# Kernel tuning notes

Measured on AMD Instinct MI355X. Metric: run time of the kernel, lower is better.

Reference implementation:

```python
import jax, jax.numpy as jnp
import numpy as np

INPUT_SIZE = 512
HIDDEN = 1024
N_QP = 64
M_QP = 128
QP_ITER = 50
MIN_EIG = 0.01
N_P = N_QP * (N_QP + 1) // 2              # 2080
N_H = M_QP * N_QP                          # 8192
N_OUT = N_P + N_QP + N_H + M_QP            # 10464
BATCH = 1024


def setup_inputs() -> dict:
    key = jax.random.key(0)
    ks = jax.random.split(key, 4)
    s = lambda fan_in: np.float32(1.0 / np.sqrt(fan_in))
    return {
        "x": jax.random.normal(ks[0], (BATCH, INPUT_SIZE), jnp.float32),
        "W1": jax.random.normal(ks[1], (INPUT_SIZE, HIDDEN), jnp.float32) * s(INPUT_SIZE),
        "b1": jnp.zeros((HIDDEN,), jnp.float32),
        "W2": jax.random.normal(ks[2], (HIDDEN, HIDDEN), jnp.float32) * s(HIDDEN),
        "b2": jnp.zeros((HIDDEN,), jnp.float32),
        "W3": jax.random.normal(ks[3], (HIDDEN, N_OUT), jnp.float32) * s(HIDDEN),
        "b3": jnp.zeros((N_OUT,), jnp.float32),
    }


def _make_psd(p):
    # p: (bs, n(n+1)/2) packed row-major lower triangle of Cholesky factor L.
    # Diagonal entries (index i(i+1)/2 - 1) -> sqrt(min_eig) + softplus, so P = L L' is PSD.
    bs = p.shape[0]
    i = jnp.arange(1, N_QP + 1)
    diag_idx = i * (i + 1) // 2 - 1
    p = p.at[:, diag_idx].set(np.float32(np.sqrt(MIN_EIG)) + jax.nn.softplus(p[:, diag_idx]))
    r, c = jnp.tril_indices(N_QP)
    L = jnp.zeros((bs, N_QP, N_QP), p.dtype).at[:, r, c].set(p)
    return jnp.einsum('bik,bjk->bij', L, L)


def _forward(x, W1, b1, W2, b2, W3, b3):
    # MLP generating QP parameters (P, q, H, b)
    h = jax.nn.relu(x @ W1 + b1)
    h = jax.nn.relu(h @ W2 + b2)
    out = h @ W3 + b3                               # (bs, N_OUT)
    P_params = out[:, :N_P]
    q = out[:, N_P:N_P + N_QP]                      # (bs, n)
    H = out[:, N_P + N_QP:N_P + N_QP + N_H].reshape(-1, M_QP, N_QP)  # (bs, m, n)
    b = out[:, N_P + N_QP + N_H:]                   # (bs, m)
    P = _make_psd(P_params)                         # (bs, n, n)

    # Step sizes: tau = sigma = 0.9 / ||H||_2, spectral norm via 10 fixed power iterations
    v = jnp.ones((x.shape[0], N_QP), x.dtype) / np.float32(np.sqrt(N_QP))
    for _ in range(10):
        w = jnp.einsum('bmn,bm->bn', H, jnp.einsum('bmn,bn->bm', H, v))
        v = w / (jnp.linalg.norm(w, axis=1, keepdims=True) + 1e-12)
    sn = jnp.linalg.norm(jnp.einsum('bmn,bn->bm', H, v), axis=1) + 1e-6
    tau = (0.9 / sn)[:, None]                       # (bs, 1) primal step
    sig = tau                                       # dual step

    # Precompute (I + tau P)^{-1} once; fixed across PDHG iterations
    eye = jnp.eye(N_QP, dtype=x.dtype)
    Minv = jnp.linalg.inv(eye[None] + tau[:, :, None] * P)

    x0 = jnp.zeros((x.shape[0], N_QP), x.dtype)
    lam0 = jnp.zeros((x.shape[0], M_QP), x.dtype)

    def step(carry, _):
        xp, xbar, lam = carry
        lam = jax.nn.relu(lam - sig * (jnp.einsum('bmn,bn->bm', H, xbar) + b))
        xn = jnp.einsum('bnk,bk->bn', Minv, xp + tau * (jnp.einsum('bmn,bm->bn', H, lam) - q))
        return (xn, 2.0 * xn - xp, lam), None

    (xs, _, _), _ = jax.lax.scan(step, (x0, x0, lam0), None, length=QP_ITER)
    return xs  # (bs, n_qp): last primal iterate, matching solver(...)[1][:, -1, :]


def reference(x, W1, b1, W2, b2, W3, b3):
    return _forward(x, W1, b1, W2, b2, W3, b3)
```

## Files before the change

### kernel.cpp

```cpp
#include <hip/hip_runtime.h>
#include <cstdint>

typedef unsigned short u16;
typedef __attribute__((ext_vector_type(8))) short short8;
typedef __attribute__((ext_vector_type(4))) float floatx4;
typedef __attribute__((ext_vector_type(4))) float f4;

#define NQP   64
#define MQP   128
#define NP    2080
#define NHH   8192
#define NOUT  10464
#define NOUTP 10496

__device__ __forceinline__ float b2f(u16 u) {
  union { unsigned int i; float f; } v; v.i = ((unsigned int)u) << 16; return v.f;
}
__device__ __forceinline__ u16 f2b(float f) {
  union { float f; unsigned int i; } v; v.f = f;
  unsigned int r = v.i + 0x7fffu + ((v.i >> 16) & 1u);
  return (u16)(r >> 16);
}

__global__ __launch_bounds__(256) void detect_dtype(const u16* __restrict__ w,
                                                    int* __restrict__ flag) {
  __shared__ int cnt;
  if (threadIdx.x == 0) cnt = 0;
  __syncthreads();
  int c = 0;
  for (int i = threadIdx.x; i < 16384; i += 256) {
    const int e = (w[i] >> 7) & 0xFF;
    if (e >= 130 || e <= 90) ++c;
  }
  atomicAdd(&cnt, c);
  __syncthreads();
  if (threadIdx.x == 0) flag[0] = (cnt > 3000) ? 1 : 0;
}

__device__ __forceinline__ u16 load_elem_bf16(const void* p, size_t idx, int isf32) {
  return isf32 ? f2b(((const float*)p)[idx]) : ((const u16*)p)[idx];
}

__global__ __launch_bounds__(256) void convert_bf16(const void* __restrict__ in,
                                                    u16* __restrict__ out, int n,
                                                    const int* __restrict__ flag) {
  const int isf = flag[0];
  for (int i = blockIdx.x * 256 + threadIdx.x; i < n; i += gridDim.x * 256)
    out[i] = load_elem_bf16(in, i, isf);
}

__global__ __launch_bounds__(256) void conv_biases(const void* __restrict__ b1,
                                                   const void* __restrict__ b2,
                                                   const void* __restrict__ b3,
                                                   float* __restrict__ bf1,
                                                   float* __restrict__ bf2,
                                                   float* __restrict__ bf3,
                                                   const int* __restrict__ flag) {
  const int isf = flag[0];
  const int i = blockIdx.x * 256 + threadIdx.x;
  if (i < 1024) {
    bf1[i] = isf ? ((const float*)b1)[i] : b2f(((const u16*)b1)[i]);
  } else if (i < 2048) {
    const int j = i - 1024;
    bf2[j] = isf ? ((const float*)b2)[j] : b2f(((const u16*)b2)[j]);
  } else if (i < 2048 + NOUT) {
    const int j = i - 2048;
    bf3[j] = isf ? ((const float*)b3)[j] : b2f(((const u16*)b3)[j]);
  }
}

__global__ __launch_bounds__(256) void transpose_all(const void* __restrict__ W1,
                                                     const void* __restrict__ W2,
                                                     const void* __restrict__ W3,
                                                     u16* __restrict__ W1t,
                                                     u16* __restrict__ W2t,
                                                     u16* __restrict__ W3t,
                                                     const int* __restrict__ flag) {
  const int bx = blockIdx.x, by = blockIdx.y;
  const void* in; u16* out; int K, N, Npad, bxo;
  if (bx < 32)      { in = W1; out = W1t; K = 512;  N = 1024; Npad = 1024;  bxo = 0;
                      if (by >= 16) return; }
  else if (bx < 64) { in = W2; out = W2t; K = 1024; N = 1024; Npad = 1024;  bxo = 32; }
  else              { in = W3; out = W3t; K = 1024; N = NOUT; Npad = NOUTP; bxo = 64; }
  __shared__ u16 tile[32][33];
  const int isf = flag[0];
  const int n0 = (bx - bxo) * 32, k0 = by * 32;
  const int tx = threadIdx.x & 31, ty = threadIdx.x >> 5;
#pragma unroll
  for (int i = 0; i < 4; ++i) {
    const int k = k0 + ty + 8 * i, n = n0 + tx;
    tile[ty + 8 * i][tx] = (n < N) ? load_elem_bf16(in, (size_t)k * N + n, isf) : (u16)0;
  }
  __syncthreads();
#pragma unroll
  for (int i = 0; i < 4; ++i) {
    const int n = n0 + ty + 8 * i, k = k0 + tx;
    if (n < Npad) out[(size_t)n * K + k] = tile[tx][ty + 8 * i];
  }
}

__device__ __forceinline__ void gload_lds16(const u16* g, u16* l) {
  __builtin_amdgcn_global_load_lds((const __attribute__((address_space(1))) void*)g,
                                   (__attribute__((address_space(3))) void*)l, 16, 0, 0);
}

template <int EPI, bool HAS_LO>
__global__ __launch_bounds__(256) void gemm_bt(const u16* __restrict__ Ahi, const u16* __restrict__ Alo,
                                               const u16* __restrict__ Bt,  const float* __restrict__ bias,
                                               u16* __restrict__ Chi, u16* __restrict__ Clo,
                                               float* __restrict__ Cf,
                                               int M, int N, int K) {
  __shared__ __align__(16) u16 lA[128 * 32];
  __shared__ __align__(16) u16 lAlo[128 * 32];
  __shared__ __align__(16) u16 lB[128 * 32];
  const int tile_n = blockIdx.x * 128;
  const int tile_m = blockIdx.y * 128;
  const int lane = threadIdx.x & 63;
  const int wv   = threadIdx.x >> 6;
  const int wm = (wv & 1) * 64;
  const int wn = (wv >> 1) * 64;
  const int sr = lane >> 2;
  const int sk = (lane & 3) * 8;
  floatx4 acc[4][4] = {};

  for (int k0 = 0; k0 < K; k0 += 32) {
#pragma unroll
    for (int it = 0; it < 2; ++it) {
      const int slot = it * 4 + wv;
      const int r = slot * 16 + sr;
      gload_lds16(Ahi + (size_t)(tile_m + r) * K + k0 + sk, lA + slot * 512);
      if (HAS_LO)
        gload_lds16(Alo + (size_t)(tile_m + r) * K + k0 + sk, lAlo + slot * 512);
      gload_lds16(Bt + (size_t)(tile_n + r) * K + k0 + sk, lB + slot * 512);
    }
    __syncthreads();
    const int ro = lane & 15;
    const int qo = (lane >> 4) * 8;
    short8 af[4], bfr[4], al[4];
#pragma unroll
    for (int i = 0; i < 4; ++i) af[i] = *(const short8*)(lA + (wm + i * 16 + ro) * 32 + qo);
#pragma unroll
    for (int j = 0; j < 4; ++j) bfr[j] = *(const short8*)(lB + (wn + j * 16 + ro) * 32 + qo);
    if (HAS_LO) {
#pragma unroll
      for (int i = 0; i < 4; ++i) al[i] = *(const short8*)(lAlo + (wm + i * 16 + ro) * 32 + qo);
    }
#pragma unroll
    for (int i = 0; i < 4; ++i)
#pragma unroll
      for (int j = 0; j < 4; ++j) {
        acc[i][j] = __builtin_amdgcn_mfma_f32_16x16x32_bf16(af[i], bfr[j], acc[i][j], 0, 0, 0);
        if (HAS_LO)
          acc[i][j] = __builtin_amdgcn_mfma_f32_16x16x32_bf16(al[i], bfr[j], acc[i][j], 0, 0, 0);
      }
    __syncthreads();
  }

  const int colb = tile_n + wn + (lane & 15);
  const int rowb = tile_m + wm + (lane >> 4) * 4;
#pragma unroll
  for (int j = 0; j < 4; ++j) {
    const int col = colb + j * 16;
    const float bv = (col < N) ? bias[col] : 0.f;
#pragma unroll
    for (int i = 0; i < 4; ++i) {
#pragma unroll
      for (int v = 0; v < 4; ++v) {
        const int row = rowb + i * 16 + v;
        float val = acc[i][j][v] + bv;
        if (EPI == 0) {
          val = fmaxf(val, 0.f);
          const u16 hi = f2b(val);
          const float lo = val - b2f(hi);
          Chi[(size_t)row * N + col] = hi;
          Clo[(size_t)row * N + col] = f2b(lo);
        } else if (EPI == 2) {
          val = fmaxf(val, 0.f);
          Chi[(size_t)row * N + col] = f2b(val);
        } else {
          if (col < N) Cf[(size_t)row * N + col] = val;
        }
      }
    }
  }
}

__device__ __forceinline__ f4 ld4s(const float* p) { return *(const f4*)p; }
__device__ __forceinline__ void st4s(float* p, f4 v) { *(f4*)p = v; }
__device__ __forceinline__ float dot4(f4 a, f4 b) {
  return fmaf(a.x, b.x, fmaf(a.y, b.y, fmaf(a.z, b.z, a.w * b.w)));
}
__device__ __forceinline__ f4 shx4(f4 v, int m) {
  f4 r;
  r.x = __shfl_xor(v.x, m, 64); r.y = __shfl_xor(v.y, m, 64);
  r.z = __shfl_xor(v.z, m, 64); r.w = __shfl_xor(v.w, m, 64);
  return r;
}
__device__ __forceinline__ int hQ(int m, int g) {
  return (m << 6) + (((g ^ (m & 15))) << 2);
}

__global__ __launch_bounds__(256, 4) void qp_solve(const float* __restrict__ outbuf,
                                                   void* __restrict__ xs,
                                                   const int* __restrict__ flag) {
  __shared__ __align__(16) float H_s[8192];
  __shared__ __align__(16) float lam_s[128];
  __shared__ __align__(16) float b_s[128];
  __shared__ __align__(16) float part_s[4][64];
  __shared__ __align__(16) float rhs_s[64];
  __shared__ __align__(16) float xb_s[64];
  __shared__ __align__(16) float xp_s[64];
  __shared__ __align__(16) float q_s[64];
  __shared__ __align__(16) float buf2[2][64];
  __shared__ float tau_sh;

  const int t = threadIdx.x;
  const int w = t >> 6, l = t & 63;
  const int am = 32 * w + (l >> 1), as = l & 1;
  const int bg = l & 15, bc = l >> 4;
  const int ci = 16 * w + (l >> 2), cc = l & 3;
  const int isf = flag[0];
  const float* ob = outbuf + (size_t)blockIdx.x * NOUT;

  float* Ld = H_s;
  float* ps = H_s + 4352;
  for (int e = t; e < 4352; e += 256) Ld[e] = 0.f;
  for (int e = t; e < NP; e += 256) ps[e] = ob[e];
  if (t < 64) q_s[t] = ob[NP + t];
  if (t >= 128 && t < 256) b_s[t - 128] = ob[NP + NQP + NHH + (t - 128)];
  __syncthreads();
  if (t < 64) {
    const int i = t + 1;
    const int d = i * (i + 1) / 2 - 1;
    const float xv = ps[d];
    ps[d] = 0.1f + (fmaxf(xv, 0.f) + log1pf(expf(-fabsf(xv))));
  }
  __syncthreads();
  for (int e = t; e < NP; e += 256) {
    int i = (int)((sqrtf(8.f * (float)e + 1.f) - 1.f) * 0.5f);
    while ((i + 1) * (i + 2) / 2 <= e) ++i;
    while (i * (i + 1) / 2 > e) --i;
    const int j = e - i * (i + 1) / 2;
    Ld[i * 68 + j] = ps[e];
  }
  __syncthreads();

  float M[16];
#pragma unroll
  for (int jj = 0; jj < 16; ++jj) M[jj] = 0.f;
#pragma unroll
  for (int h = 0; h < 2; ++h) {
    f4 Lr[8];
#pragma unroll
    for (int g = 0; g < 8; ++g) Lr[g] = ld4s(&Ld[ci * 68 + (h * 8 + g) * 4]);
#pragma unroll
    for (int jj = 0; jj < 16; ++jj) {
      const int j = 16 * cc + jj;
      float s = 0.f;
#pragma unroll
      for (int g = 0; g < 8; ++g) s += dot4(Lr[g], ld4s(&Ld[j * 68 + (h * 8 + g) * 4]));
      M[jj] += s;
    }
  }
  __syncthreads();

  for (int e = t; e < NHH; e += 256) {
    const int m = e >> 6, n = e & 63;
    H_s[hQ(m, n >> 2) + (n & 3)] = ob[NP + NQP + e];
  }
  if (t < 64) xb_s[t] = 0.125f;
  __syncthreads();

  for (int pi = 0; pi < 10; ++pi) {
    {
      float s = 0.f;
#pragma unroll
      for (int k = 0; k < 8; ++k) {
        const int g = 8 * as + k;
        s += dot4(ld4s(&H_s[hQ(am, g)]), ld4s(&xb_s[4 * g]));
      }
      s += __shfl_xor(s, 1, 64);
      if (as == 0) lam_s[am] = s;
    }
    __syncthreads();
    {
      f4 u = {0.f, 0.f, 0.f, 0.f};
#pragma unroll
      for (int k = 0; k < 8; ++k) {
        const int m = 32 * w + 8 * bc + k;
        u += ld4s(&H_s[hQ(m, bg)]) * lam_s[m];
      }
      u += shx4(u, 16); u += shx4(u, 32);
      if (l < 16) st4s(&part_s[w][4 * bg], u);
    }
    __syncthreads();
    if (t < 64) {
      const float u = part_s[0][t] + part_s[1][t] + part_s[2][t] + part_s[3][t];
      float ss = u * u;
#pragma unroll
      for (int o = 1; o <= 32; o <<= 1) ss += __shfl_xor(ss, o, 64);
      xb_s[t] = u / (sqrtf(ss) + 1e-12f);
    }
    __syncthreads();
  }
  {
    float s = 0.f;
#pragma unroll
    for (int k = 0; k < 8; ++k) {
      const int g = 8 * as + k;
      s += dot4(ld4s(&H_s[hQ(am, g)]), ld4s(&xb_s[4 * g]));
    }
    s += __shfl_xor(s, 1, 64);
    if (as == 0) lam_s[am] = s;
  }
  __syncthreads();
  if (t < 64) {
    const float a = lam_s[t], bb = lam_s[t + 64];
    float ss = a * a + bb * bb;
#pragma unroll
    for (int o = 1; o <= 32; o <<= 1) ss += __shfl_xor(ss, o, 64);
    if (t == 0) tau_sh = 0.9f / (sqrtf(ss) + 1e-6f);
  }
  __syncthreads();
  const float tau = tau_sh;

#pragma unroll
  for (int jj = 0; jj < 16; ++jj)
    M[jj] = tau * M[jj] + ((16 * cc + jj == ci) ? 1.0f : 0.0f);

  if (ci == 0) {
#pragma unroll
    for (int jj = 0; jj < 16; ++jj) buf2[0][16 * cc + jj] = M[jj];
  }
  __syncthreads();
#pragma unroll
  for (int k = 0; k < 64; ++k) {
    const int kb = k & 1;
    const int kc = k >> 4;
    const float d = 1.0f / buf2[kb][k];
    f4 rv[4];
#pragma unroll
    for (int u = 0; u < 4; ++u) rv[u] = ld4s(&buf2[kb][16 * cc + 4 * u]);
    const float f = __shfl(M[k & 15], (l & 60) | kc, 64);
    if (ci == k) {
#pragma unroll
      for (int jj = 0; jj < 16; ++jj) M[jj] = rv[jj >> 2][jj & 3] * d;
      if (cc == kc) M[k & 15] = d;
    } else {
#pragma unroll
      for (int jj = 0; jj < 16; ++jj)
        M[jj] = fmaf(-f, rv[jj >> 2][jj & 3] * d, M[jj]);
      if (cc == kc) M[k & 15] = -f * d;
    }
    if (k < 63 && ci == k + 1) {
#pragma unroll
      for (int jj = 0; jj < 16; ++jj) buf2[1 - kb][16 * cc + jj] = M[jj];
    }
    __syncthreads();
  }

  float c0;
  {
    float acc = 0.f;
#pragma unroll
    for (int u = 0; u < 4; ++u) {
      const f4 qv = ld4s(&q_s[16 * cc + 4 * u]);
      acc = fmaf(M[4 * u + 0], qv.x, acc);
      acc = fmaf(M[4 * u + 1], qv.y, acc);
      acc = fmaf(M[4 * u + 2], qv.z, acc);
      acc = fmaf(M[4 * u + 3], qv.w, acc);
    }
    acc += __shfl_xor(acc, 1, 64);
    acc += __shfl_xor(acc, 2, 64);
    c0 = tau * acc;
  }

  if (t < 64) { xb_s[t] = 0.f; xp_s[t] = 0.f; }
  float lam = 0.f, xpr = 0.f;
  const float br = b_s[am];
  __syncthreads();

  for (int it = 0; it < 50; ++it) {
    {
      float s = 0.f;
#pragma unroll
      for (int k = 0; k < 8; ++k) {
        const int g = 8 * as + k;
        s += dot4(ld4s(&H_s[hQ(am, g)]), ld4s(&xb_s[4 * g]));
      }
      s += __shfl_xor(s, 1, 64);
      lam = fmaxf(lam - tau * (s + br), 0.f);
      if (as == 0) lam_s[am] = lam;
    }
    __syncthreads();
    {
      f4 u = {0.f, 0.f, 0.f, 0.f};
#pragma unroll
      for (int k = 0; k < 8; ++k) {
        const int m = 32 * w + 8 * bc + k;
        u += ld4s(&H_s[hQ(m, bg)]) * lam_s[m];
      }
      u += shx4(u, 16); u += shx4(u, 32);
      if (l < 16) st4s(&part_s[w][4 * bg], u);
    }
    __syncthreads();
    if (t < 64) {
      const float uu = part_s[0][t] + part_s[1][t] + part_s[2][t] + part_s[3][t];
      rhs_s[t] = xp_s[t] + tau * uu;
    }
    __syncthreads();
    {
      float acc = 0.f;
#pragma unroll
      for (int u = 0; u < 4; ++u) {
        const f4 rv = ld4s(&rhs_s[16 * cc + 4 * u]);
        acc = fmaf(M[4 * u + 0], rv.x, acc);
        acc = fmaf(M[4 * u + 1], rv.y, acc);
        acc = fmaf(M[4 * u + 2], rv.z, acc);
        acc = fmaf(M[4 * u + 3], rv.w, acc);
      }
      acc += __shfl_xor(acc, 1, 64);
      acc += __shfl_xor(acc, 2, 64);
      if (cc == 0) {
        const float xn = acc - c0;
        xp_s[ci] = xn;
        xb_s[ci] = 2.f * xn - xpr;
        xpr = xn;
      }
    }
    __syncthreads();
  }

  if (cc == 0) {
    const size_t oi = (size_t)blockIdx.x * NQP + ci;
    if (isf) ((float*)xs)[oi] = xpr;
    else     ((u16*)xs)[oi]   = f2b(xpr);
  }
}

extern "C" void kernel_launch(void* const* d_in, const int* in_sizes, int n_in,
                              void* d_out, int out_size, void* d_ws, size_t ws_size,
                              hipStream_t stream) {
  const void* x  = d_in[0];
  const void* W1 = d_in[1];
  const void* b1 = d_in[2];
  const void* W2 = d_in[3];
  const void* b2 = d_in[4];
  const void* W3 = d_in[5];
  const void* b3 = d_in[6];

  char* ws = (char*)d_ws;
  size_t off = 0;
  auto take = [&](size_t bytes) -> char* {
    char* r = ws + off;
    off += (bytes + 255) & ~(size_t)255;
    return r;
  };
  int*   flag = (int*)take(256);
  float* bf1  = (float*)take(1024 * 4);
  float* bf2  = (float*)take(1024 * 4);
  float* bf3  = (float*)take((size_t)NOUT * 4);
  u16*   W3t  = (u16*)take((size_t)NOUTP * 1024 * 2);
  u16*   h2hi = (u16*)take(1024ull * 1024 * 2);
  char*  region = take(1024ull * NOUT * 4);
  float* outf = (float*)region;
  u16* xb   = (u16*)(region + 0);
  u16* W1t  = (u16*)(region + (1u << 20));
  u16* W2t  = (u16*)(region + (2u << 20));
  u16* h1hi = (u16*)(region + (4u << 20));
  u16* h1lo = (u16*)(region + (6u << 20));
  (void)ws_size; (void)in_sizes; (void)n_in; (void)out_size;

  detect_dtype<<<dim3(1), 256, 0, stream>>>((const u16*)W1, flag);

  convert_bf16<<<dim3(512), 256, 0, stream>>>(x, xb, 1024 * 512, flag);
  conv_biases<<<dim3(49), 256, 0, stream>>>(b1, b2, b3, bf1, bf2, bf3, flag);
  transpose_all<<<dim3(392, 32), 256, 0, stream>>>(W1, W2, W3, W1t, W2t, W3t, flag);

  gemm_bt<0, false><<<dim3(8, 8), 256, 0, stream>>>(xb, nullptr, W1t, bf1,
                                                    h1hi, h1lo, nullptr, 1024, 1024, 512);
  gemm_bt<2, true><<<dim3(8, 8), 256, 0, stream>>>(h1hi, h1lo, W2t, bf2,
                                                   h2hi, nullptr, nullptr, 1024, 1024, 1024);
  gemm_bt<1, false><<<dim3(NOUTP / 128, 8), 256, 0, stream>>>(h2hi, nullptr, W3t, bf3,
                                                              nullptr, nullptr, outf, 1024, NOUT, 1024);
  qp_solve<<<dim3(1024), 256, 0, stream>>>(outf, d_out, flag);
}
```

Measured before the change: 488.9 us.

## Keep H in registers, use readlane broadcast, cut PDHG barriers per iteration

Each thread now holds its H row slice and an H column slice in registers instead of staging all of H in shared memory. Lambda values are broadcast across the wave with readlane rather than through shared memory. The rhs reduction is folded into the M-multiply step, and xp is double-buffered so each PDHG iteration needs two barriers instead of four. This lowers LDS traffic, shared-memory footprint and sync overhead, at the cost of about 64 more VGPRs per thread, which could hurt occupancy under launch_bounds(256,4).

```diff
diff --git a/kernel.cpp b/kernel.cpp
--- a/kernel.cpp
+++ b/kernel.cpp
@@ -186,48 +186,37 @@
 }
 
 __device__ __forceinline__ f4 ld4s(const float* p) { return *(const f4*)p; }
-__device__ __forceinline__ void st4s(float* p, f4 v) { *(f4*)p = v; }
 __device__ __forceinline__ float dot4(f4 a, f4 b) {
   return fmaf(a.x, b.x, fmaf(a.y, b.y, fmaf(a.z, b.z, a.w * b.w)));
 }
-__device__ __forceinline__ f4 shx4(f4 v, int m) {
-  f4 r;
-  r.x = __shfl_xor(v.x, m, 64); r.y = __shfl_xor(v.y, m, 64);
-  r.z = __shfl_xor(v.z, m, 64); r.w = __shfl_xor(v.w, m, 64);
-  return r;
-}
-__device__ __forceinline__ int hQ(int m, int g) {
-  return (m << 6) + (((g ^ (m & 15))) << 2);
+__device__ __forceinline__ float rdlane(float v, int lane) {
+  return __int_as_float(__builtin_amdgcn_readlane(__float_as_int(v), lane));
 }
 
 __global__ __launch_bounds__(256, 4) void qp_solve(const float* __restrict__ outbuf,
                                                    void* __restrict__ xs,
                                                    const int* __restrict__ flag) {
-  __shared__ __align__(16) float H_s[8192];
-  __shared__ __align__(16) float lam_s[128];
-  __shared__ __align__(16) float b_s[128];
+  __shared__ __align__(16) float LS[6432];
   __shared__ __align__(16) float part_s[4][64];
-  __shared__ __align__(16) float rhs_s[64];
   __shared__ __align__(16) float xb_s[64];
-  __shared__ __align__(16) float xp_s[64];
+  __shared__ __align__(16) float xp_s[2][64];
   __shared__ __align__(16) float q_s[64];
   __shared__ __align__(16) float buf2[2][64];
-  __shared__ float tau_sh;
 
   const int t = threadIdx.x;
   const int w = t >> 6, l = t & 63;
-  const int am = 32 * w + (l >> 1), as = l & 1;
-  const int bg = l & 15, bc = l >> 4;
+  const int as = l & 1;
+  const int am = 32 * w + (l >> 1);
   const int ci = 16 * w + (l >> 2), cc = l & 3;
   const int isf = flag[0];
   const float* ob = outbuf + (size_t)blockIdx.x * NOUT;
-
-  float* Ld = H_s;
-  float* ps = H_s + 4352;
+  const float* Hg = ob + (NP + NQP);
+
+  float* Ld = LS;
+  float* ps = LS + 4352;
   for (int e = t; e < 4352; e += 256) Ld[e] = 0.f;
   for (int e = t; e < NP; e += 256) ps[e] = ob[e];
   if (t < 64) q_s[t] = ob[NP + t];
-  if (t >= 128 && t < 256) b_s[t - 128] = ob[NP + NQP + NHH + (t - 128)];
   __syncthreads();
   if (t < 64) {
     const int i = t + 1;
@@ -262,67 +251,64 @@
       M[jj] += s;
     }
   }
-  __syncthreads();
-
-  for (int e = t; e < NHH; e += 256) {
-    const int m = e >> 6, n = e & 63;
-    H_s[hQ(m, n >> 2) + (n & 3)] = ob[NP + NQP + e];
-  }
+
+  f4 hrow[8];
+#pragma unroll
+  for (int k = 0; k < 8; ++k)
+    hrow[k] = ld4s(Hg + (size_t)am * 64 + as * 32 + k * 4);
+  float hcol[32];
+#pragma unroll
+  for (int j = 0; j < 32; ++j) hcol[j] = Hg[(32 * w + j) * 64 + l];
+  const float br = ob[NP + NQP + NHH + am];
+
   if (t < 64) xb_s[t] = 0.125f;
   __syncthreads();
 
   for (int pi = 0; pi < 10; ++pi) {
-    {
-      float s = 0.f;
-#pragma unroll
-      for (int k = 0; k < 8; ++k) {
-        const int g = 8 * as + k;
-        s += dot4(ld4s(&H_s[hQ(am, g)]), ld4s(&xb_s[4 * g]));
-      }
-      s += __shfl_xor(s, 1, 64);
-      if (as == 0) lam_s[am] = s;
-    }
-    __syncthreads();
-    {
-      f4 u = {0.f, 0.f, 0.f, 0.f};
-#pragma unroll
-      for (int k = 0; k < 8; ++k) {
-        const int m = 32 * w + 8 * bc + k;
-        u += ld4s(&H_s[hQ(m, bg)]) * lam_s[m];
-      }
-      u += shx4(u, 16); u += shx4(u, 32);
-      if (l < 16) st4s(&part_s[w][4 * bg], u);
-    }
-    __syncthreads();
-    if (t < 64) {
-      const float u = part_s[0][t] + part_s[1][t] + part_s[2][t] + part_s[3][t];
-      float ss = u * u;
-#pragma unroll
-      for (int o = 1; o <= 32; o <<= 1) ss += __shfl_xor(ss, o, 64);
-      xb_s[t] = u / (sqrtf(ss) + 1e-12f);
-    }
-    __syncthreads();
-  }
+    float s0 = 0.f, s1 = 0.f;
+#pragma unroll
+    for (int k = 0; k < 8; k += 2) {
+      s0 += dot4(hrow[k],     ld4s(&xb_s[4 * (8 * as + k)]));
+      s1 += dot4(hrow[k + 1], ld4s(&xb_s[4 * (8 * as + k + 1)]));
+    }
+    float s = s0 + s1;
+    s += __shfl_xor(s, 1, 64);
+    float u0 = 0.f, u1 = 0.f, u2 = 0.f, u3 = 0.f;
+#pragma unroll
+    for (int j = 0; j < 8; ++j) {
+      u0 = fmaf(hcol[4 * j + 0], rdlane(s, 8 * j + 0), u0);
+      u1 = fmaf(hcol[4 * j + 1], rdlane(s, 8 * j + 2), u1);
+      u2 = fmaf(hcol[4 * j + 2], rdlane(s, 8 * j + 4), u2);
+      u3 = fmaf(hcol[4 * j + 3], rdlane(s, 8 * j + 6), u3);
+    }
+    part_s[w][l] = (u0 + u1) + (u2 + u3);
+    __syncthreads();
+    const float ut = (part_s[0][l] + part_s[1][l]) + (part_s[2][l] + part_s[3][l]);
+    float ss = ut * ut;
+#pragma unroll
+    for (int o = 1; o <= 32; o <<= 1) ss += __shfl_xor(ss, o, 64);
+    const float vn = ut / (sqrtf(ss) + 1e-12f);
+    if (w == 0) xb_s[l] = vn;
+    __syncthreads();
+  }
+
+  float tau;
   {
-    float s = 0.f;
-#pragma unroll
-    for (int k = 0; k < 8; ++k) {
-      const int g = 8 * as + k;
-      s += dot4(ld4s(&H_s[hQ(am, g)]), ld4s(&xb_s[4 * g]));
-    }
+    float s0 = 0.f, s1 = 0.f;
+#pragma unroll
+    for (int k = 0; k < 8; k += 2) {
+      s0 += dot4(hrow[k],     ld4s(&xb_s[4 * (8 * as + k)]));
+      s1 += dot4(hrow[k + 1], ld4s(&xb_s[4 * (8 * as + k + 1)]));
+    }
+    float s = s0 + s1;
     s += __shfl_xor(s, 1, 64);
-    if (as == 0) lam_s[am] = s;
-  }
-  __syncthreads();
-  if (t < 64) {
-    const float a = lam_s[t], bb = lam_s[t + 64];
-    float ss = a * a + bb * bb;
+    float ss = as ? 0.f : s * s;
 #pragma unroll
     for (int o = 1; o <= 32; o <<= 1) ss += __shfl_xor(ss, o, 64);
-    if (t == 0) tau_sh = 0.9f / (sqrtf(ss) + 1e-6f);
-  }
-  __syncthreads();
-  const float tau = tau_sh;
+    if (l == 0) part_s[w][0] = ss;
+  }
+  __syncthreads();
+  tau = 0.9f / (sqrtf(part_s[0][0] + part_s[1][0] + part_s[2][0] + part_s[3][0]) + 1e-6f);
 
 #pragma unroll
   for (int jj = 0; jj < 16; ++jj)
@@ -375,58 +361,50 @@
     c0 = tau * acc;
   }
 
-  if (t < 64) { xb_s[t] = 0.f; xp_s[t] = 0.f; }
+  if (t < 64) { xb_s[t] = 0.f; xp_s[0][t] = 0.f; }
   float lam = 0.f, xpr = 0.f;
-  const float br = b_s[am];
   __syncthreads();
 
   for (int it = 0; it < 50; ++it) {
-    {
-      float s = 0.f;
-#pragma unroll
-      for (int k = 0; k < 8; ++k) {
-        const int g = 8 * as + k;
-        s += dot4(ld4s(&H_s[hQ(am, g)]), ld4s(&xb_s[4 * g]));
-      }
-      s += __shfl_xor(s, 1, 64);
-      lam = fmaxf(lam - tau * (s + br), 0.f);
-      if (as == 0) lam_s[am] = lam;
-    }
-    __syncthreads();
-    {
-      f4 u = {0.f, 0.f, 0.f, 0.f};
-#pragma unroll
-      for (int k = 0; k < 8; ++k) {
-        const int m = 32 * w + 8 * bc + k;
-        u += ld4s(&H_s[hQ(m, bg)]) * lam_s[m];
-      }
-      u += shx4(u, 16); u += shx4(u, 32);
-      if (l < 16) st4s(&part_s[w][4 * bg], u);
-    }
-    __syncthreads();
-    if (t < 64) {
-      const float uu = part_s[0][t] + part_s[1][t] + part_s[2][t] + part_s[3][t];
-      rhs_s[t] = xp_s[t] + tau * uu;
-    }
-    __syncthreads();
-    {
-      float acc = 0.f;
-#pragma unroll
-      for (int u = 0; u < 4; ++u) {
-        const f4 rv = ld4s(&rhs_s[16 * cc + 4 * u]);
-        acc = fmaf(M[4 * u + 0], rv.x, acc);
-        acc = fmaf(M[4 * u + 1], rv.y, acc);
-        acc = fmaf(M[4 * u + 2], rv.z, acc);
-        acc = fmaf(M[4 * u + 3], rv.w, acc);
-      }
-      acc += __shfl_xor(acc, 1, 64);
-      acc += __shfl_xor(acc, 2, 64);
-      if (cc == 0) {
-        const float xn = acc - c0;
-        xp_s[ci] = xn;
-        xb_s[ci] = 2.f * xn - xpr;
-        xpr = xn;
-      }
+    float s0 = 0.f, s1 = 0.f;
+#pragma unroll
+    for (int k = 0; k < 8; k += 2) {
+      s0 += dot4(hrow[k],     ld4s(&xb_s[4 * (8 * as + k)]));
+      s1 += dot4(hrow[k + 1], ld4s(&xb_s[4 * (8 * as + k + 1)]));
+    }
+    float s = s0 + s1;
+    s += __shfl_xor(s, 1, 64);
+    lam = fmaxf(lam - tau * (s + br), 0.f);
+    float u0 = 0.f, u1 = 0.f, u2 = 0.f, u3 = 0.f;
+#pragma unroll
+    for (int j = 0; j < 8; ++j) {
+      u0 = fmaf(hcol[4 * j + 0], rdlane(lam, 8 * j + 0), u0);
+      u1 = fmaf(hcol[4 * j + 1], rdlane(lam, 8 * j + 2), u1);
+      u2 = fmaf(hcol[4 * j + 2], rdlane(lam, 8 * j + 4), u2);
+      u3 = fmaf(hcol[4 * j + 3], rdlane(lam, 8 * j + 6), u3);
+    }
+    part_s[w][l] = (u0 + u1) + (u2 + u3);
+    __syncthreads();
+    const float* xrd = xp_s[it & 1];
+    float acc = 0.f;
+#pragma unroll
+    for (int u = 0; u < 4; ++u) {
+      const int base = 16 * cc + 4 * u;
+      f4 pv = (ld4s(&part_s[0][base]) + ld4s(&part_s[1][base])) +
+              (ld4s(&part_s[2][base]) + ld4s(&part_s[3][base]));
+      f4 rv = ld4s(&xrd[base]) + pv * tau;
+      acc = fmaf(M[4 * u + 0], rv.x, acc);
+      acc = fmaf(M[4 * u + 1], rv.y, acc);
+      acc = fmaf(M[4 * u + 2], rv.z, acc);
+      acc = fmaf(M[4 * u + 3], rv.w, acc);
+    }
+    acc += __shfl_xor(acc, 1, 64);
+    acc += __shfl_xor(acc, 2, 64);
+    if (cc == 0) {
+      const float xn = acc - c0;
+      xp_s[1 - (it & 1)][ci] = xn;
+      xb_s[ci] = 2.f * xn - xpr;
+      xpr = xn;
     }
     __syncthreads();
   }
```

Result: slower. 1.223 ms (+150.1%).

## Cut per-iteration barriers in QP solver via lane shuffles and redundant reductions

Applied to the files above, without the earlier changes.

In both the power iteration and the PDHG loop, the lambda vector now reaches the H^T·lam product through wavefront shuffles instead of a shared-memory round trip, which removes one barrier per iteration. Every thread now sums the four partial buffers itself, removing the separate rhs stage and its barrier. Double-buffering xp avoids a read/write race, and the tau reduction is merged into the per-wave sums. The cost is extra redundant LDS reads and shuffles in exchange for fewer __syncthreads in the serial 60-iteration chain.

```diff
diff --git a/kernel.cpp b/kernel.cpp
--- a/kernel.cpp
+++ b/kernel.cpp
@@ -204,20 +204,18 @@
                                                    void* __restrict__ xs,
                                                    const int* __restrict__ flag) {
   __shared__ __align__(16) float H_s[8192];
-  __shared__ __align__(16) float lam_s[128];
   __shared__ __align__(16) float b_s[128];
   __shared__ __align__(16) float part_s[4][64];
-  __shared__ __align__(16) float rhs_s[64];
   __shared__ __align__(16) float xb_s[64];
-  __shared__ __align__(16) float xp_s[64];
+  __shared__ __align__(16) float xp_s[2][64];
   __shared__ __align__(16) float q_s[64];
   __shared__ __align__(16) float buf2[2][64];
-  __shared__ float tau_sh;
 
   const int t = threadIdx.x;
   const int w = t >> 6, l = t & 63;
   const int am = 32 * w + (l >> 1), as = l & 1;
   const int bg = l & 15, bc = l >> 4;
+  const int bb2 = l & 48;
   const int ci = 16 * w + (l >> 2), cc = l & 3;
   const int isf = flag[0];
   const float* ob = outbuf + (size_t)blockIdx.x * NOUT;
@@ -272,37 +270,32 @@
   __syncthreads();
 
   for (int pi = 0; pi < 10; ++pi) {
-    {
-      float s = 0.f;
-#pragma unroll
-      for (int k = 0; k < 8; ++k) {
-        const int g = 8 * as + k;
-        s += dot4(ld4s(&H_s[hQ(am, g)]), ld4s(&xb_s[4 * g]));
-      }
-      s += __shfl_xor(s, 1, 64);
-      if (as == 0) lam_s[am] = s;
-    }
-    __syncthreads();
+    float s = 0.f;
+#pragma unroll
+    for (int k = 0; k < 8; ++k) {
+      const int g = 8 * as + k;
+      s += dot4(ld4s(&H_s[hQ(am, g)]), ld4s(&xb_s[4 * g]));
+    }
+    s += __shfl_xor(s, 1, 64);
     {
       f4 u = {0.f, 0.f, 0.f, 0.f};
 #pragma unroll
       for (int k = 0; k < 8; ++k) {
         const int m = 32 * w + 8 * bc + k;
-        u += ld4s(&H_s[hQ(m, bg)]) * lam_s[m];
+        u += ld4s(&H_s[hQ(m, bg)]) * __shfl(s, bb2 + 2 * k, 64);
       }
       u += shx4(u, 16); u += shx4(u, 32);
       if (l < 16) st4s(&part_s[w][4 * bg], u);
     }
     __syncthreads();
-    if (t < 64) {
-      const float u = part_s[0][t] + part_s[1][t] + part_s[2][t] + part_s[3][t];
-      float ss = u * u;
-#pragma unroll
-      for (int o = 1; o <= 32; o <<= 1) ss += __shfl_xor(ss, o, 64);
-      xb_s[t] = u / (sqrtf(ss) + 1e-12f);
-    }
-    __syncthreads();
-  }
+    const float ut = (part_s[0][l] + part_s[1][l]) + (part_s[2][l] + part_s[3][l]);
+    float ss = ut * ut;
+#pragma unroll
+    for (int o = 1; o <= 32; o <<= 1) ss += __shfl_xor(ss, o, 64);
+    if (w == 0) xb_s[l] = ut / (sqrtf(ss) + 1e-12f);
+    __syncthreads();
+  }
+
   {
     float s = 0.f;
 #pragma unroll
@@ -311,18 +304,13 @@
       s += dot4(ld4s(&H_s[hQ(am, g)]), ld4s(&xb_s[4 * g]));
     }
     s += __shfl_xor(s, 1, 64);
-    if (as == 0) lam_s[am] = s;
-  }
-  __syncthreads();
-  if (t < 64) {
-    const float a = lam_s[t], bb = lam_s[t + 64];
-    float ss = a * a + bb * bb;
+    float ss = as ? 0.f : s * s;
 #pragma unroll
     for (int o = 1; o <= 32; o <<= 1) ss += __shfl_xor(ss, o, 64);
-    if (t == 0) tau_sh = 0.9f / (sqrtf(ss) + 1e-6f);
-  }
-  __syncthreads();
-  const float tau = tau_sh;
+    if (l == 0) part_s[w][0] = ss;
+  }
+  __syncthreads();
+  const float tau = 0.9f / (sqrtf(part_s[0][0] + part_s[1][0] + part_s[2][0] + part_s[3][0]) + 1e-6f);
 
 #pragma unroll
   for (int jj = 0; jj < 16; ++jj)
@@ -375,58 +363,52 @@
     c0 = tau * acc;
   }
 
-  if (t < 64) { xb_s[t] = 0.f; xp_s[t] = 0.f; }
+  if (t < 64) { xb_s[t] = 0.f; xp_s[0][t] = 0.f; }
   float lam = 0.f, xpr = 0.f;
   const float br = b_s[am];
   __syncthreads();
 
   for (int it = 0; it < 50; ++it) {
-    {
-      float s = 0.f;
-#pragma unroll
-      for (int k = 0; k < 8; ++k) {
-        const int g = 8 * as + k;
-        s += dot4(ld4s(&H_s[hQ(am, g)]), ld4s(&xb_s[4 * g]));
-      }
-      s += __shfl_xor(s, 1, 64);
-      lam = fmaxf(lam - tau * (s + br), 0.f);
-      if (as == 0) lam_s[am] = lam;
-    }
-    __syncthreads();
+    float s = 0.f;
+#pragma unroll
+    for (int k = 0; k < 8; ++k) {
+      const int g = 8 * as + k;
+      s += dot4(ld4s(&H_s[hQ(am, g)]), ld4s(&xb_s[4 * g]));
+    }
+    s += __shfl_xor(s, 1, 64);
+    lam = fmaxf(lam - tau * (s + br), 0.f);
     {
       f4 u = {0.f, 0.f, 0.f, 0.f};
 #pragma unroll
       for (int k = 0; k < 8; ++k) {
         const int m = 32 * w + 8 * bc + k;
-        u += ld4s(&H_s[hQ(m, bg)]) * lam_s[m];
+        u += ld4s(&H_s[hQ(m, bg)]) * __shfl(lam, bb2 + 2 * k, 64);
       }
       u += shx4(u, 16); u += shx4(u, 32);
       if (l < 16) st4s(&part_s[w][4 * bg], u);
     }
     __syncthreads();
-    if (t < 64) {
-      const float uu = part_s[0][t] + part_s[1][t] + part_s[2][t] + part_s[3][t];
-      rhs_s[t] = xp_s[t] + tau * uu;
-    }
-    __syncthreads();
-    {
-      float acc = 0.f;
-#pragma unroll
-      for (int u = 0; u < 4; ++u) {
-        const f4 rv = ld4s(&rhs_s[16 * cc + 4 * u]);
-        acc = fmaf(M[4 * u + 0], rv.x, acc);
-        acc = fmaf(M[4 * u + 1], rv.y, acc);
-        acc = fmaf(M[4 * u + 2], rv.z, acc);
-        acc = fmaf(M[4 * u + 3], rv.w, acc);
-      }
-      acc += __shfl_xor(acc, 1, 64);
-      acc += __shfl_xor(acc, 2, 64);
-      if (cc == 0) {
-        const float xn = acc - c0;
-        xp_s[ci] = xn;
-        xb_s[ci] = 2.f * xn - xpr;
-        xpr = xn;
-      }
+    const float* xrd = xp_s[it & 1];
+    float* xwr = xp_s[1 - (it & 1)];
+    float acc = 0.f;
+#pragma unroll
+    for (int u = 0; u < 4; ++u) {
+      const int base = 16 * cc + 4 * u;
+      const f4 pv = (ld4s(&part_s[0][base]) + ld4s(&part_s[1][base])) +
+                    (ld4s(&part_s[2][base]) + ld4s(&part_s[3][base]));
+      const f4 rv = ld4s(&xrd[base]) + pv * tau;
+      acc = fmaf(M[4 * u + 0], rv.x, acc);
+      acc = fmaf(M[4 * u + 1], rv.y, acc);
+      acc = fmaf(M[4 * u + 2], rv.z, acc);
+      acc = fmaf(M[4 * u + 3], rv.w, acc);
+    }
+    acc += __shfl_xor(acc, 1, 64);
+    acc += __shfl_xor(acc, 2, 64);
+    if (cc == 0) {
+      const float xn = acc - c0;
+      xwr[ci] = xn;
+      xb_s[ci] = 2.f * xn - xpr;
+      xpr = xn;
     }
     __syncthreads();
   }
```

Result: slower. 511.4 us (+4.6%).
